# Performance work log

Hardware: AMD Instinct MI355X
Metric: run time of the kernel (lower is better)

## Reference

```python
import jax, jax.numpy as jnp
import numpy as np

EPS = 1e-07
NUM_ITERATIONS = 3

B, O, H, W, I, D = 8, 32, 14, 14, 32, 16


def squash(s, axis=-1):
    # squared norm over capsule dim
    sq = jnp.sum(s * s, axis=axis)                      # [..., ] norms
    safe = jnp.sqrt(sq + EPS)
    factor = sq / (1.0 + sq)
    return (factor / safe)[..., None] * s


def setup_inputs() -> dict:
    key = jax.random.key(0)
    k1, = jax.random.split(key, 1)
    preds = jax.random.normal(k1, (B, O, H, W, I, D), dtype=jnp.float32)
    b = jnp.zeros((1, O, H, W, I), dtype=jnp.float32)   # routing logits param
    return {"tensor_of_prediction_vector": preds, "b": b}


def reference(tensor_of_prediction_vector, b):
    preds = tensor_of_prediction_vector                 # [B,O,H,W,I,D]
    c = jax.nn.softmax(b, axis=-1)                      # [1,O,H,W,I]
    v = squash(jnp.sum(c[..., None] * preds, axis=-2))  # [B,O,H,W,D]
    b_batch = b
    for _ in range(NUM_ITERATIONS):
        # agreement: dot(pred, v) over capsule dim -> [B,O,H,W,I]
        b_batch = b_batch + jnp.sum(preds * v[..., None, :], axis=-1)
        c = jax.nn.softmax(b_batch, axis=-1)
        v = squash(jnp.sum(preds * c[..., None], axis=-2))
    return v
```

## Files before the change

### kernel.cpp

```cpp
#include <hip/hip_runtime.h>


#define EPSQ 1e-7f

constexpr int NI = 32, ND = 16;
constexpr int SITES = 50176;
constexpr int OHW   = 6272;
constexpr int THREADS = 256;
constexpr int BLOCKS  = SITES * 4 / THREADS;

__device__ __forceinline__ float dpp_xor1(float x) {
    return __int_as_float(__builtin_amdgcn_mov_dpp(__float_as_int(x), 0xB1, 0xF, 0xF, true));
}
__device__ __forceinline__ float dpp_xor2(float x) {
    return __int_as_float(__builtin_amdgcn_mov_dpp(__float_as_int(x), 0x4E, 0xF, 0xF, true));
}

__device__ __forceinline__ void fma4(float4& a, float c, const float4& x) {
    a.x = fmaf(c, x.x, a.x); a.y = fmaf(c, x.y, a.y);
    a.z = fmaf(c, x.z, a.z); a.w = fmaf(c, x.w, a.w);
}
__device__ __forceinline__ float dot4(const float4& a, const float4& b) {
    return fmaf(a.x, b.x, fmaf(a.y, b.y, fmaf(a.z, b.z, a.w * b.w)));
}
__device__ __forceinline__ void qred4(float4& a) {
    a.x += dpp_xor1(a.x); a.y += dpp_xor1(a.y);
    a.z += dpp_xor1(a.z); a.w += dpp_xor1(a.w);
    a.x += dpp_xor2(a.x); a.y += dpp_xor2(a.y);
    a.z += dpp_xor2(a.z); a.w += dpp_xor2(a.w);
}

__global__ __launch_bounds__(256, 2) void routing_kernel(
    const float* __restrict__ preds,
    const float* __restrict__ bparam,
    float* __restrict__ out)
{
    const int tid  = blockIdx.x * THREADS + threadIdx.x;
    const int site = tid >> 2;
    const int q    = tid & 3;

    const float4* pb = (const float4*)(preds + (size_t)site * (NI * ND) + q * (8 * ND));
    float4 p[8][4];
    #pragma unroll
    for (int k = 0; k < 8; ++k)
        #pragma unroll
        for (int j = 0; j < 4; ++j)
            p[k][j] = pb[k * 4 + j];

    const int sohw = site % OHW;
    const float4* bb = (const float4*)(bparam + (size_t)sohw * NI + q * 8);
    float bl[8];
    {
        float4 t0 = bb[0], t1 = bb[1];
        bl[0] = t0.x; bl[1] = t0.y; bl[2] = t0.z; bl[3] = t0.w;
        bl[4] = t1.x; bl[5] = t1.y; bl[6] = t1.z; bl[7] = t1.w;
    }

    float4 v0, v1, v2, v3;

    auto pass = [&]() {
        float m = bl[0];
        #pragma unroll
        for (int k = 1; k < 8; ++k) m = fmaxf(m, bl[k]);
        m = fmaxf(m, dpp_xor1(m));
        m = fmaxf(m, dpp_xor2(m));
        float e[8];
        float sm = 0.0f;
        #pragma unroll
        for (int k = 0; k < 8; ++k) { e[k] = __expf(bl[k] - m); sm += e[k]; }
        sm += dpp_xor1(sm);
        sm += dpp_xor2(sm);
        const float r = __frcp_rn(sm);

        float4 s0 = {0,0,0,0}, s1 = {0,0,0,0}, s2 = {0,0,0,0}, s3 = {0,0,0,0};
        #pragma unroll
        for (int k = 0; k < 8; ++k) {
            fma4(s0, e[k], p[k][0]);
            fma4(s1, e[k], p[k][1]);
            fma4(s2, e[k], p[k][2]);
            fma4(s3, e[k], p[k][3]);
        }
        qred4(s0); qred4(s1); qred4(s2); qred4(s3);
        s0.x *= r; s0.y *= r; s0.z *= r; s0.w *= r;
        s1.x *= r; s1.y *= r; s1.z *= r; s1.w *= r;
        s2.x *= r; s2.y *= r; s2.z *= r; s2.w *= r;
        s3.x *= r; s3.y *= r; s3.z *= r; s3.w *= r;

        const float sq = dot4(s0, s0) + dot4(s1, s1) + dot4(s2, s2) + dot4(s3, s3);
        const float t  = sq / ((1.0f + sq) * sqrtf(sq + EPSQ));
        v0.x = t * s0.x; v0.y = t * s0.y; v0.z = t * s0.z; v0.w = t * s0.w;
        v1.x = t * s1.x; v1.y = t * s1.y; v1.z = t * s1.z; v1.w = t * s1.w;
        v2.x = t * s2.x; v2.y = t * s2.y; v2.z = t * s2.z; v2.w = t * s2.w;
        v3.x = t * s3.x; v3.y = t * s3.y; v3.z = t * s3.z; v3.w = t * s3.w;
    };

    pass();

    #pragma unroll
    for (int it = 0; it < 3; ++it) {
        #pragma unroll
        for (int k = 0; k < 8; ++k) {
            bl[k] += dot4(p[k][0], v0) + dot4(p[k][1], v1)
                   + dot4(p[k][2], v2) + dot4(p[k][3], v3);
        }
        pass();
    }

    const float4 w = (q == 0) ? v0 : (q == 1) ? v1 : (q == 2) ? v2 : v3;
    *(float4*)(out + (size_t)site * ND + q * 4) = w;
}

extern "C" void kernel_launch(void* const* d_in, const int* in_sizes, int n_in,
                              void* d_out, int out_size, void* d_ws, size_t ws_size,
                              hipStream_t stream) {
    const float* preds  = (const float*)d_in[0];
    const float* bparam = (const float*)d_in[1];
    float* out = (float*)d_out;
    routing_kernel<<<BLOCKS, THREADS, 0, stream>>>(preds, bparam, out);
}
```

Baseline: 33.81 us.

## Coalesce prediction loads through per-wave LDS transpose and simplify softmax/squash math

Each wave now loads its 16 sites' predictions with fully coalesced float4 loads. The data is staged through a swizzled 16KB-per-wave LDS buffer and transposed into the per-thread register layout the routing loop already uses. The goal is to replace strided 512-byte-per-lane global accesses with contiguous ones. Softmax drops the max-subtraction, and squash folds the normalization into one scale using reciprocal and rsqrt intrinsics. In exchange, the block needs 64KB of LDS, and exp can overflow if the routing logits grow large.

```diff
diff --git a/kernel.cpp b/kernel.cpp
--- a/kernel.cpp
+++ b/kernel.cpp
@@ -7,7 +7,7 @@
 constexpr int SITES = 50176;
 constexpr int OHW   = 6272;
 constexpr int THREADS = 256;
-constexpr int BLOCKS  = SITES * 4 / THREADS;
+constexpr int BLOCKS  = SITES / 64;
 
 __device__ __forceinline__ float dpp_xor1(float x) {
     return __int_as_float(__builtin_amdgcn_mov_dpp(__float_as_int(x), 0xB1, 0xF, 0xF, true));
@@ -15,7 +15,6 @@
 __device__ __forceinline__ float dpp_xor2(float x) {
     return __int_as_float(__builtin_amdgcn_mov_dpp(__float_as_int(x), 0x4E, 0xF, 0xF, true));
 }
-
 __device__ __forceinline__ void fma4(float4& a, float c, const float4& x) {
     a.x = fmaf(c, x.x, a.x); a.y = fmaf(c, x.y, a.y);
     a.z = fmaf(c, x.z, a.z); a.w = fmaf(c, x.w, a.w);
@@ -35,39 +34,69 @@
     const float* __restrict__ bparam,
     float* __restrict__ out)
 {
-    const int tid  = blockIdx.x * THREADS + threadIdx.x;
-    const int site = tid >> 2;
-    const int q    = tid & 3;
+    __shared__ float4 lds4[4096];
+    const int tid  = threadIdx.x;
+    const int lane = tid & 63;
+    const int wib  = tid >> 6;
+    const int wave = blockIdx.x * 4 + wib;
+    const int q    = lane & 3;
+    const int s_w  = lane >> 2;
+    const int site = wave * 16 + s_w;
 
-    const float4* pb = (const float4*)(preds + (size_t)site * (NI * ND) + q * (8 * ND));
-    float4 p[8][4];
+    float4* wlds = lds4 + wib * 1024;
+    const float4* pg = (const float4*)preds + (size_t)wave * 2048;
+
+    float4 t0[16], t1[16];
     #pragma unroll
-    for (int k = 0; k < 8; ++k)
-        #pragma unroll
-        for (int j = 0; j < 4; ++j)
-            p[k][j] = pb[k * 4 + j];
+    for (int k = 0; k < 16; ++k) t0[k] = pg[k * 64 + lane];
+    #pragma unroll
+    for (int k = 0; k < 16; ++k) t1[k] = pg[1024 + k * 64 + lane];
 
     const int sohw = site % OHW;
-    const float4* bb = (const float4*)(bparam + (size_t)sohw * NI + q * 8);
-    float bl[8];
-    {
-        float4 t0 = bb[0], t1 = bb[1];
-        bl[0] = t0.x; bl[1] = t0.y; bl[2] = t0.z; bl[3] = t0.w;
-        bl[4] = t1.x; bl[5] = t1.y; bl[6] = t1.z; bl[7] = t1.w;
+    const float4* bb4 = (const float4*)(bparam + (size_t)sohw * NI + q * 8);
+    const float4 bA = bb4[0], bB = bb4[1];
+    float bl[8] = {bA.x, bA.y, bA.z, bA.w, bB.x, bB.y, bB.z, bB.w};
+
+    float4 p[8][4];
+    const int cb = 32 * q;
+
+    #pragma unroll
+    for (int k = 0; k < 16; ++k) {
+        const int x = k >> 1;
+        wlds[x * 128 + ((((k & 1) * 64) + lane) ^ x)] = t0[k];
+    }
+    asm volatile("s_waitcnt lgkmcnt(0)" ::: "memory");
+    if (s_w < 8) {
+        const int x = s_w;
+        #pragma unroll
+        for (int r = 0; r < 8; ++r)
+            #pragma unroll
+            for (int u = 0; u < 4; ++u)
+                p[r][u] = wlds[x * 128 + ((cb + 4 * r + u) ^ x)];
+    }
+    asm volatile("s_waitcnt lgkmcnt(0)" ::: "memory");
+    #pragma unroll
+    for (int k = 0; k < 16; ++k) {
+        const int x = k >> 1;
+        wlds[x * 128 + ((((k & 1) * 64) + lane) ^ x)] = t1[k];
+    }
+    asm volatile("s_waitcnt lgkmcnt(0)" ::: "memory");
+    if (s_w >= 8) {
+        const int x = s_w - 8;
+        #pragma unroll
+        for (int r = 0; r < 8; ++r)
+            #pragma unroll
+            for (int u = 0; u < 4; ++u)
+                p[r][u] = wlds[x * 128 + ((cb + 4 * r + u) ^ x)];
     }
 
     float4 v0, v1, v2, v3;
 
     auto pass = [&]() {
-        float m = bl[0];
-        #pragma unroll
-        for (int k = 1; k < 8; ++k) m = fmaxf(m, bl[k]);
-        m = fmaxf(m, dpp_xor1(m));
-        m = fmaxf(m, dpp_xor2(m));
         float e[8];
         float sm = 0.0f;
         #pragma unroll
-        for (int k = 0; k < 8; ++k) { e[k] = __expf(bl[k] - m); sm += e[k]; }
+        for (int k = 0; k < 8; ++k) { e[k] = __expf(bl[k]); sm += e[k]; }
         sm += dpp_xor1(sm);
         sm += dpp_xor2(sm);
         const float r = __frcp_rn(sm);
@@ -75,23 +104,18 @@
         float4 s0 = {0,0,0,0}, s1 = {0,0,0,0}, s2 = {0,0,0,0}, s3 = {0,0,0,0};
         #pragma unroll
         for (int k = 0; k < 8; ++k) {
-            fma4(s0, e[k], p[k][0]);
-            fma4(s1, e[k], p[k][1]);
-            fma4(s2, e[k], p[k][2]);
-            fma4(s3, e[k], p[k][3]);
+            fma4(s0, e[k], p[k][0]); fma4(s1, e[k], p[k][1]);
+            fma4(s2, e[k], p[k][2]); fma4(s3, e[k], p[k][3]);
         }
         qred4(s0); qred4(s1); qred4(s2); qred4(s3);
-        s0.x *= r; s0.y *= r; s0.z *= r; s0.w *= r;
-        s1.x *= r; s1.y *= r; s1.z *= r; s1.w *= r;
-        s2.x *= r; s2.y *= r; s2.z *= r; s2.w *= r;
-        s3.x *= r; s3.y *= r; s3.z *= r; s3.w *= r;
 
-        const float sq = dot4(s0, s0) + dot4(s1, s1) + dot4(s2, s2) + dot4(s3, s3);
-        const float t  = sq / ((1.0f + sq) * sqrtf(sq + EPSQ));
-        v0.x = t * s0.x; v0.y = t * s0.y; v0.z = t * s0.z; v0.w = t * s0.w;
-        v1.x = t * s1.x; v1.y = t * s1.y; v1.z = t * s1.z; v1.w = t * s1.w;
-        v2.x = t * s2.x; v2.y = t * s2.y; v2.z = t * s2.z; v2.w = t * s2.w;
-        v3.x = t * s3.x; v3.y = t * s3.y; v3.z = t * s3.z; v3.w = t * s3.w;
+        const float sqt = dot4(s0, s0) + dot4(s1, s1) + dot4(s2, s2) + dot4(s3, s3);
+        const float sq  = r * r * sqt;
+        const float f   = sq * __frcp_rn(1.0f + sq) * __frsqrt_rn(sq + EPSQ) * r;
+        v0.x = f*s0.x; v0.y = f*s0.y; v0.z = f*s0.z; v0.w = f*s0.w;
+        v1.x = f*s1.x; v1.y = f*s1.y; v1.z = f*s1.z; v1.w = f*s1.w;
+        v2.x = f*s2.x; v2.y = f*s2.y; v2.z = f*s2.z; v2.w = f*s2.w;
+        v3.x = f*s3.x; v3.y = f*s3.y; v3.z = f*s3.z; v3.w = f*s3.w;
     };
 
     pass();
@@ -106,8 +130,8 @@
         pass();
     }
 
-    const float4 w = (q == 0) ? v0 : (q == 1) ? v1 : (q == 2) ? v2 : v3;
-    *(float4*)(out + (size_t)site * ND + q * 4) = w;
+    float4 w = (q == 0) ? v0 : (q == 1) ? v1 : (q == 2) ? v2 : v3;
+    ((float4*)out)[(size_t)site * 4 + q] = w;
 }
 
 extern "C" void kernel_launch(void* const* d_in, const int* in_sizes, int n_in,
```

New measurement: 27.64 us. 18.3% less time.
